# Kernel tuning notes

Hardware: AMD Instinct MI355X
Metric: run time of the kernel (lower is better)

## Reference

```python
import jax, jax.numpy as jnp
import numpy as np

N_NODES = 100_000
N_EDGES = 1_600_000
F_IN, F_HID, F_OUT = 128, 64, 128


def setup_inputs() -> dict:
    key = jax.random.key(0)
    k_x, k_e, k_w1, k_w2 = jax.random.split(key, 4)
    x = jax.random.normal(k_x, (N_NODES, F_IN), dtype=jnp.float32)
    edge_index = jax.random.randint(k_e, (2, N_EDGES), 0, N_NODES, dtype=jnp.int32)
    # Glorot-style init for the two GCN conv weight matrices
    W1 = jax.random.normal(k_w1, (F_IN, F_HID), dtype=jnp.float32) * (1.0 / np.sqrt(F_IN))
    b1 = jnp.zeros((F_HID,), dtype=jnp.float32)
    W2 = jax.random.normal(k_w2, (F_HID, F_OUT), dtype=jnp.float32) * (1.0 / np.sqrt(F_HID))
    b2 = jnp.zeros((F_OUT,), dtype=jnp.float32)
    return {"x": x, "edge_index": edge_index, "W1": W1, "b1": b1, "W2": W2, "b2": b2}


def _gcn_conv(x, W, b, src, dst, num_nodes):
    """GCNConv: out = D^{-1/2} (A + I) D^{-1/2} (x W) + b.
    Self-loops handled analytically: deg includes +1, and the self-loop
    message for node i is norm_i^2 * h_i."""
    h = x @ W  # [N, F_out]
    ones = jnp.ones(src.shape[0], dtype=h.dtype)
    deg = jax.ops.segment_sum(ones, dst, num_segments=num_nodes) + 1.0  # +1 self-loop
    norm = jax.lax.rsqrt(deg)  # [N]
    # gather source messages scaled by norm_src, scatter-add into dst
    agg = jax.ops.segment_sum(h[src] * norm[src, None], dst, num_segments=num_nodes)
    return norm[:, None] * agg + (norm * norm)[:, None] * h + b


def reference(x, edge_index, W1, b1, W2, b2):
    src, dst = edge_index[0], edge_index[1]
    n = x.shape[0]
    h = jax.nn.relu(_gcn_conv(x, W1, b1, src, dst, n))
    # dropout p=0.0 -> identity (module default)
    return _gcn_conv(h, W2, b2, src, dst, n)
```

## Files before the change

### kernel.cpp

```cpp
#include <hip/hip_runtime.h>
#include <hip/hip_bf16.h>

#define F_IN 128
#define F_HID 64
#define F_OUT 128
#define BSH 9
#define BS  (1 << BSH)
#define MAXNB 256

__device__ __forceinline__ int clampi(int v, int lo, int hi) {
    return v < lo ? lo : (v > hi ? hi : v);
}

__device__ __forceinline__ unsigned short f2bf(float f) {
    unsigned int u = __float_as_uint(f);
    u = (u + 0x7FFFu + ((u >> 16) & 1u)) >> 16;
    return (unsigned short)u;
}
__device__ __forceinline__ float bf2f(unsigned short s) {
    return __uint_as_float(((unsigned int)s) << 16);
}

__global__ void zero2_kernel(int* __restrict__ a, int* __restrict__ b, int n) {
    int i = blockIdx.x * blockDim.x + threadIdx.x;
    if (i < n) { a[i] = 0; b[i] = 0; }
}

__global__ void bhist_kernel(const int* __restrict__ dst, int* __restrict__ bhist,
                             int E, int Nn, int NB) {
    __shared__ int lh[MAXNB];
    for (int i = threadIdx.x; i < NB; i += 256) lh[i] = 0;
    __syncthreads();
    int chunk = (E + gridDim.x - 1) / gridDim.x;
    int base = blockIdx.x * chunk;
    int end = base + chunk; if (end > E) end = E;
    for (int i = base + threadIdx.x; i < end; i += 256) {
        int d = clampi(dst[i], 0, Nn - 1);
        atomicAdd(&lh[d >> BSH], 1);
    }
    __syncthreads();
    for (int i = threadIdx.x; i < NB; i += 256)
        if (lh[i]) atomicAdd(&bhist[i], lh[i]);
}

__global__ void bscan_kernel(const int* __restrict__ bhist, int* __restrict__ bbase, int NB) {
    __shared__ int s[MAXNB];
    int t = threadIdx.x;
    int v = (t < NB) ? bhist[t] : 0;
    s[t] = v;
    __syncthreads();
    for (int d = 1; d < MAXNB; d <<= 1) {
        int x = (t >= d) ? s[t - d] : 0;
        __syncthreads();
        s[t] += x;
        __syncthreads();
    }
    if (t < NB) bbase[t] = s[t] - v;
}

__global__ void bplace_kernel(const int* __restrict__ src, const int* __restrict__ dst,
                              const int* __restrict__ bbase, int* __restrict__ bcur,
                              int* __restrict__ staging, int E, int Nn, int NB) {
    __shared__ int lh[MAXNB];
    __shared__ int gb[MAXNB];
    for (int i = threadIdx.x; i < NB; i += 256) lh[i] = 0;
    __syncthreads();
    int chunk = (E + gridDim.x - 1) / gridDim.x;
    int base = blockIdx.x * chunk;
    int end = base + chunk; if (end > E) end = E;
    for (int i = base + threadIdx.x; i < end; i += 256) {
        int d = clampi(dst[i], 0, Nn - 1);
        atomicAdd(&lh[d >> BSH], 1);
    }
    __syncthreads();
    for (int i = threadIdx.x; i < NB; i += 256) {
        int c = lh[i];
        gb[i] = (c > 0) ? bbase[i] + atomicAdd(&bcur[i], c) : 0;
        lh[i] = 0;
    }
    __syncthreads();
    for (int i = base + threadIdx.x; i < end; i += 256) {
        int d = clampi(dst[i], 0, Nn - 1);
        int s = clampi(src[i], 0, Nn - 1);
        int b = d >> BSH;
        int p = gb[b] + atomicAdd(&lh[b], 1);
        staging[p] = (s << BSH) | (d & (BS - 1));
    }
}

__global__ void bfine_kernel(const int* __restrict__ bhist, const int* __restrict__ bbase,
                             const int* __restrict__ staging,
                             int* __restrict__ cnt, int* __restrict__ off,
                             float* __restrict__ nrm, int* __restrict__ csr, int Nn) {
    __shared__ int lcnt[BS];
    __shared__ int loff[BS];
    __shared__ int lcur[BS];
    __shared__ int ps[256];
    int b = blockIdx.x;
    int t = threadIdx.x;
    int base  = bbase[b];
    int count = bhist[b];
    int node0 = b << BSH;

    for (int r = t; r < BS; r += 256) lcnt[r] = 0;
    __syncthreads();
    for (int i = t; i < count; i += 256)
        atomicAdd(&lcnt[staging[base + i] & (BS - 1)], 1);
    __syncthreads();

    int a0 = lcnt[2 * t], a1 = lcnt[2 * t + 1];
    int pair = a0 + a1;
    ps[t] = pair;
    __syncthreads();
    for (int d = 1; d < 256; d <<= 1) {
        int x = (t >= d) ? ps[t - d] : 0;
        __syncthreads();
        ps[t] += x;
        __syncthreads();
    }
    int excl = ps[t] - pair;
    loff[2 * t]     = excl;
    loff[2 * t + 1] = excl + a0;
    __syncthreads();

    for (int r = t; r < BS; r += 256) {
        int node = node0 + r;
        if (node < Nn) {
            int c = lcnt[r];
            cnt[node] = c;
            off[node] = base + loff[r];
            nrm[node] = rsqrtf((float)c + 1.0f);
        }
        lcur[r] = 0;
    }
    __syncthreads();

    for (int i = t; i < count; i += 256) {
        int v = staging[base + i];
        int r = v & (BS - 1);
        int p = base + loff[r] + atomicAdd(&lcur[r], 1);
        csr[p] = v >> BSH;
    }
}

template<int K, int N, bool PRESCALE, bool BIAS, bool BF16OUT>
__global__ void gemm_tiled(const float* __restrict__ A, const float* __restrict__ B,
                           const float* __restrict__ nrm, const float* __restrict__ bias,
                           void* __restrict__ Cv, int M) {
    constexpr int CT = N / 8;
    constexpr int RB = (256 / CT) * 4;
    __shared__ float Ws[K * N];

    int tid = threadIdx.x;
    for (int i = tid; i < K * N / 4; i += 256)
        ((float4*)Ws)[i] = ((const float4*)B)[i];
    __syncthreads();

    int ct = tid % CT;
    int rt = tid / CT;
    int row0 = blockIdx.x * RB + rt * 4;
    int c0 = ct * 8;

    float acc[4][8];
#pragma unroll
    for (int r = 0; r < 4; r++)
#pragma unroll
        for (int c = 0; c < 8; c++) acc[r][c] = 0.f;

    for (int kk = 0; kk < K; kk += 8) {
        float4 av[4], av2[4];
#pragma unroll
        for (int r = 0; r < 4; r++) {
            int row = row0 + r;
            if (row < M) {
                av[r]  = *(const float4*)(A + (size_t)row * K + kk);
                av2[r] = *(const float4*)(A + (size_t)row * K + kk + 4);
            } else {
                av[r]  = make_float4(0.f, 0.f, 0.f, 0.f);
                av2[r] = make_float4(0.f, 0.f, 0.f, 0.f);
            }
        }
#pragma unroll
        for (int j = 0; j < 4; j++) {
            const float* wrow = Ws + (kk + j) * N + c0;
            float4 w0 = *(const float4*)(wrow);
            float4 w1 = *(const float4*)(wrow + 4);
            float wj[8] = {w0.x, w0.y, w0.z, w0.w, w1.x, w1.y, w1.z, w1.w};
#pragma unroll
            for (int r = 0; r < 4; r++) {
                float a = (j == 0) ? av[r].x : (j == 1) ? av[r].y : (j == 2) ? av[r].z : av[r].w;
#pragma unroll
                for (int c = 0; c < 8; c++)
                    acc[r][c] = fmaf(a, wj[c], acc[r][c]);
            }
        }
#pragma unroll
        for (int j = 0; j < 4; j++) {
            const float* wrow = Ws + (kk + 4 + j) * N + c0;
            float4 w0 = *(const float4*)(wrow);
            float4 w1 = *(const float4*)(wrow + 4);
            float wj[8] = {w0.x, w0.y, w0.z, w0.w, w1.x, w1.y, w1.z, w1.w};
#pragma unroll
            for (int r = 0; r < 4; r++) {
                float a = (j == 0) ? av2[r].x : (j == 1) ? av2[r].y : (j == 2) ? av2[r].z : av2[r].w;
#pragma unroll
                for (int c = 0; c < 8; c++)
                    acc[r][c] = fmaf(a, wj[c], acc[r][c]);
            }
        }
    }

    float bcol[8];
    if (BIAS) {
        float4 bb0 = *(const float4*)(bias + c0);
        float4 bb1 = *(const float4*)(bias + c0 + 4);
        bcol[0]=bb0.x; bcol[1]=bb0.y; bcol[2]=bb0.z; bcol[3]=bb0.w;
        bcol[4]=bb1.x; bcol[5]=bb1.y; bcol[6]=bb1.z; bcol[7]=bb1.w;
    }

#pragma unroll
    for (int r = 0; r < 4; r++) {
        int row = row0 + r;
        if (row >= M) continue;
        float scale = PRESCALE ? nrm[row] : 1.0f;
        float o[8];
#pragma unroll
        for (int c = 0; c < 8; c++) {
            float v = acc[r][c];
            if (PRESCALE) v *= scale;
            if (BIAS)     v += bcol[c];
            o[c] = v;
        }
        if (BF16OUT) {
            unsigned int pk0 = (unsigned int)f2bf(o[0]) | ((unsigned int)f2bf(o[1]) << 16);
            unsigned int pk1 = (unsigned int)f2bf(o[2]) | ((unsigned int)f2bf(o[3]) << 16);
            unsigned int pk2 = (unsigned int)f2bf(o[4]) | ((unsigned int)f2bf(o[5]) << 16);
            unsigned int pk3 = (unsigned int)f2bf(o[6]) | ((unsigned int)f2bf(o[7]) << 16);
            uint4 pk; pk.x = pk0; pk.y = pk1; pk.z = pk2; pk.w = pk3;
            *(uint4*)((unsigned short*)Cv + (size_t)row * N + c0) = pk;
        } else {
            float4 o0, o1;
            o0.x = o[0]; o0.y = o[1]; o0.z = o[2]; o0.w = o[3];
            o1.x = o[4]; o1.y = o[5]; o1.z = o[6]; o1.w = o[7];
            float* crow = (float*)Cv + (size_t)row * N + c0;
            *(float4*)(crow) = o0;
            *(float4*)(crow + 4) = o1;
        }
    }
}

template<bool CONV>
__global__ void gather64_kernel(const unsigned short* __restrict__ h,
                                const float* __restrict__ norm,
                                const int* __restrict__ off, const int* __restrict__ cnt,
                                const int* __restrict__ csr_src,
                                const float* __restrict__ bias,
                                void* __restrict__ outv, int Nn, int E) {
    int wave = (blockIdx.x * blockDim.x + threadIdx.x) >> 6;
    int lane = threadIdx.x & 63;
    int node = __builtin_amdgcn_readfirstlane(wave);
    if (node >= Nn) return;

    int o0 = __builtin_amdgcn_readfirstlane(off[node]);
    int c  = __builtin_amdgcn_readfirstlane(cnt[node]);
    if (c < 0) c = 0;
    if (o0 < 0) o0 = 0;
    if (o0 + c > E) c = E - o0;

    const int* ce = csr_src + o0;
    float sum = 0.0f;
    int e = 0;
    for (; e + 16 <= c; e += 16) {
        int si[16];
        unsigned short v[16];
#pragma unroll
        for (int u = 0; u < 16; u++) si[u] = clampi(ce[e + u], 0, Nn - 1);
#pragma unroll
        for (int u = 0; u < 16; u++) v[u] = h[(size_t)si[u] * 64 + lane];
#pragma unroll
        for (int u = 0; u < 16; u++) sum += bf2f(v[u]);
    }
    for (; e + 8 <= c; e += 8) {
        int si[8];
        unsigned short v[8];
#pragma unroll
        for (int u = 0; u < 8; u++) si[u] = clampi(ce[e + u], 0, Nn - 1);
#pragma unroll
        for (int u = 0; u < 8; u++) v[u] = h[(size_t)si[u] * 64 + lane];
#pragma unroll
        for (int u = 0; u < 8; u++) sum += bf2f(v[u]);
    }
    for (; e + 4 <= c; e += 4) {
        int si[4];
        unsigned short v[4];
#pragma unroll
        for (int u = 0; u < 4; u++) si[u] = clampi(ce[e + u], 0, Nn - 1);
#pragma unroll
        for (int u = 0; u < 4; u++) v[u] = h[(size_t)si[u] * 64 + lane];
#pragma unroll
        for (int u = 0; u < 4; u++) sum += bf2f(v[u]);
    }
    for (; e < c; e++) {
        int s = clampi(ce[e], 0, Nn - 1);
        sum += bf2f(h[(size_t)s * 64 + lane]);
    }
    float self = bf2f(h[(size_t)node * 64 + lane]);
    float nv = norm[node];
    float r = nv * (sum + self);
    if (CONV) {
        r = nv * fmaxf(r + bias[lane], 0.0f);
        ((unsigned short*)outv)[(size_t)node * 64 + lane] = f2bf(r);
    } else {
        ((float*)outv)[(size_t)node * 64 + lane] = r;
    }
}

extern "C" void kernel_launch(void* const* d_in, const int* in_sizes, int n_in,
                              void* d_out, int out_size, void* d_ws, size_t ws_size,
                              hipStream_t stream) {
    if (n_in < 6) return;
    const float* x   = (const float*)d_in[0];
    const int*   ei  = (const int*)d_in[1];
    const float* W1  = (const float*)d_in[2];
    const float* b1  = (const float*)d_in[3];
    const float* W2  = (const float*)d_in[4];
    const float* b2  = (const float*)d_in[5];
    float*       out = (float*)d_out;

    int Nn = in_sizes[0] / F_IN;
    int E  = in_sizes[1] / 2;
    const int* src = ei;
    const int* dst = ei + E;

    int NB = (Nn + BS - 1) >> BSH;
    if (NB > MAXNB) return;
    if (Nn > (1 << (31 - BSH))) return;

    size_t o = 0;
    auto alloc = [&](size_t bytes) { size_t cur = o; o += (bytes + 255) & ~(size_t)255; return cur; };
    size_t o_cnt   = alloc((size_t)Nn * 4);
    size_t o_off   = alloc((size_t)Nn * 4);
    size_t o_nrm   = alloc((size_t)Nn * 4);
    size_t o_csr   = alloc((size_t)E * 4);
    size_t o_stg   = alloc((size_t)E * 4);
    size_t o_bh    = alloc(MAXNB * 4);
    size_t o_bb    = alloc(MAXNB * 4);
    size_t o_bc    = alloc(MAXNB * 4);
    size_t o_h     = alloc((size_t)Nn * F_HID * 4);
    if (o > ws_size) return;

    char* ws = (char*)d_ws;
    int*   cnt   = (int*)(ws + o_cnt);
    int*   off   = (int*)(ws + o_off);
    float* nrm   = (float*)(ws + o_nrm);
    int*   csr   = (int*)(ws + o_csr);
    int*   stg   = (int*)(ws + o_stg);
    int*   bh    = (int*)(ws + o_bh);
    int*   bb    = (int*)(ws + o_bb);
    int*   bc    = (int*)(ws + o_bc);
    unsigned short* h1 = (unsigned short*)(ws + o_h);
    float*          q  = (float*)(ws + o_h);
    unsigned short* p  = (unsigned short*)(out + (size_t)Nn * F_HID);

    zero2_kernel<<<1, 256, 0, stream>>>(bh, bc, MAXNB);
    bhist_kernel<<<256, 256, 0, stream>>>(dst, bh, E, Nn, NB);
    bscan_kernel<<<1, 256, 0, stream>>>(bh, bb, NB);
    bplace_kernel<<<256, 256, 0, stream>>>(src, dst, bb, bc, stg, E, Nn, NB);
    bfine_kernel<<<NB, 256, 0, stream>>>(bh, bb, stg, cnt, off, nrm, csr, Nn);

    {
        constexpr int RB = (256 / (F_HID / 8)) * 4;
        gemm_tiled<F_IN, F_HID, true, false, true><<<(Nn + RB - 1) / RB, 256, 0, stream>>>(
            x, W1, nrm, nullptr, h1, Nn);
    }
    gather64_kernel<true><<<(Nn + 3) / 4, 256, 0, stream>>>(
        h1, nrm, off, cnt, csr, b1, p, Nn, E);

    gather64_kernel<false><<<(Nn + 3) / 4, 256, 0, stream>>>(
        p, nrm, off, cnt, csr, nullptr, q, Nn, E);
    {
        constexpr int RB = (256 / (F_OUT / 8)) * 4;
        gemm_tiled<F_HID, F_OUT, false, true, false><<<(Nn + RB - 1) / RB, 256, 0, stream>>>(
            q, W2, nullptr, b2, out, Nn);
    }
}
```

Before: 331.3 us.

## Fuse second-layer aggregation with W2 projection in one persistent kernel

The second gather and the following 64x128 GEMM are merged into one persistent kernel. It stages W2 in shared memory and computes each aggregated row's projection right after gathering it. This removes the fp32 intermediate write and re-read of q and one kernel launch. The cost is a 32KB shared-memory footprint per block, which limits occupancy for the latency-bound gather. The GEMM also becomes a per-node FMA loop with a fixed grid of 1024 blocks, and p moves into the workspace.

```diff
diff --git a/kernel.cpp b/kernel.cpp
--- a/kernel.cpp
+++ b/kernel.cpp
@@ -249,13 +249,12 @@
     }
 }
 
-template<bool CONV>
 __global__ void gather64_kernel(const unsigned short* __restrict__ h,
                                 const float* __restrict__ norm,
                                 const int* __restrict__ off, const int* __restrict__ cnt,
                                 const int* __restrict__ csr_src,
                                 const float* __restrict__ bias,
-                                void* __restrict__ outv, int Nn, int E) {
+                                unsigned short* __restrict__ outp, int Nn, int E) {
     int wave = (blockIdx.x * blockDim.x + threadIdx.x) >> 6;
     int lane = threadIdx.x & 63;
     int node = __builtin_amdgcn_readfirstlane(wave);
@@ -307,11 +306,104 @@
     float self = bf2f(h[(size_t)node * 64 + lane]);
     float nv = norm[node];
     float r = nv * (sum + self);
-    if (CONV) {
-        r = nv * fmaxf(r + bias[lane], 0.0f);
-        ((unsigned short*)outv)[(size_t)node * 64 + lane] = f2bf(r);
-    } else {
-        ((float*)outv)[(size_t)node * 64 + lane] = r;
+    r = nv * fmaxf(r + bias[lane], 0.0f);
+    outp[(size_t)node * 64 + lane] = f2bf(r);
+}
+
+__global__ void gather_w2_kernel(const unsigned short* __restrict__ p,
+                                 const float* __restrict__ norm,
+                                 const int* __restrict__ off, const int* __restrict__ cnt,
+                                 const int* __restrict__ csr_src,
+                                 const float* __restrict__ W2,
+                                 const float* __restrict__ b2,
+                                 float* __restrict__ out, int Nn, int E) {
+    __shared__ float W2s[F_HID * F_OUT];
+    __shared__ float qs[4][F_HID];
+
+    int tid = threadIdx.x;
+    for (int i = tid; i < F_HID * F_OUT / 4; i += 256)
+        ((float4*)W2s)[i] = ((const float4*)W2)[i];
+    __syncthreads();
+
+    int lane = tid & 63;
+    int wv   = tid >> 6;
+    int half = lane >> 5;
+    int c4   = (lane & 31) * 4;
+    int kb   = half * 32;
+
+    float4 breg = *(const float4*)(b2 + c4);
+
+    int wave0  = (blockIdx.x * blockDim.x + tid) >> 6;
+    int nwaves = (gridDim.x * blockDim.x) >> 6;
+
+    for (int node = wave0; node < Nn; node += nwaves) {
+        int un = __builtin_amdgcn_readfirstlane(node);
+        int o0 = __builtin_amdgcn_readfirstlane(off[un]);
+        int c  = __builtin_amdgcn_readfirstlane(cnt[un]);
+        if (c < 0) c = 0;
+        if (o0 < 0) o0 = 0;
+        if (o0 + c > E) c = E - o0;
+
+        const int* ce = csr_src + o0;
+        float sum = 0.0f;
+        int e = 0;
+        for (; e + 8 <= c; e += 8) {
+            int si[8];
+            unsigned short v[8];
+#pragma unroll
+            for (int u = 0; u < 8; u++) si[u] = clampi(ce[e + u], 0, Nn - 1);
+#pragma unroll
+            for (int u = 0; u < 8; u++) v[u] = p[(size_t)si[u] * 64 + lane];
+#pragma unroll
+            for (int u = 0; u < 8; u++) sum += bf2f(v[u]);
+        }
+        for (; e + 4 <= c; e += 4) {
+            int si[4];
+            unsigned short v[4];
+#pragma unroll
+            for (int u = 0; u < 4; u++) si[u] = clampi(ce[e + u], 0, Nn - 1);
+#pragma unroll
+            for (int u = 0; u < 4; u++) v[u] = p[(size_t)si[u] * 64 + lane];
+#pragma unroll
+            for (int u = 0; u < 4; u++) sum += bf2f(v[u]);
+        }
+        for (; e < c; e++) {
+            int s = clampi(ce[e], 0, Nn - 1);
+            sum += bf2f(p[(size_t)s * 64 + lane]);
+        }
+        float self = bf2f(p[(size_t)un * 64 + lane]);
+        float q = norm[un] * (sum + self);
+        qs[wv][lane] = q;
+
+        float4 acc = make_float4(0.f, 0.f, 0.f, 0.f);
+#pragma unroll
+        for (int kc = 0; kc < 32; kc += 4) {
+            float4 qv = *(const float4*)(&qs[wv][kb + kc]);
+            const float* wr = W2s + (size_t)(kb + kc) * F_OUT + c4;
+            float4 w0 = *(const float4*)(wr);
+            float4 w1 = *(const float4*)(wr + F_OUT);
+            float4 w2 = *(const float4*)(wr + 2 * F_OUT);
+            float4 w3 = *(const float4*)(wr + 3 * F_OUT);
+            acc.x = fmaf(qv.x, w0.x, acc.x); acc.y = fmaf(qv.x, w0.y, acc.y);
+            acc.z = fmaf(qv.x, w0.z, acc.z); acc.w = fmaf(qv.x, w0.w, acc.w);
+            acc.x = fmaf(qv.y, w1.x, acc.x); acc.y = fmaf(qv.y, w1.y, acc.y);
+            acc.z = fmaf(qv.y, w1.z, acc.z); acc.w = fmaf(qv.y, w1.w, acc.w);
+            acc.x = fmaf(qv.z, w2.x, acc.x); acc.y = fmaf(qv.z, w2.y, acc.y);
+            acc.z = fmaf(qv.z, w2.z, acc.z); acc.w = fmaf(qv.z, w2.w, acc.w);
+            acc.x = fmaf(qv.w, w3.x, acc.x); acc.y = fmaf(qv.w, w3.y, acc.y);
+            acc.z = fmaf(qv.w, w3.z, acc.z); acc.w = fmaf(qv.w, w3.w, acc.w);
+        }
+
+        float ox = acc.x + __shfl_down(acc.x, 32);
+        float oy = acc.y + __shfl_down(acc.y, 32);
+        float oz = acc.z + __shfl_down(acc.z, 32);
+        float ow = acc.w + __shfl_down(acc.w, 32);
+        if (half == 0) {
+            float4 o;
+            o.x = ox + breg.x; o.y = oy + breg.y;
+            o.z = oz + breg.z; o.w = ow + breg.w;
+            *(float4*)(out + (size_t)un * F_OUT + c4) = o;
+        }
     }
 }
 
@@ -359,8 +451,7 @@
     int*   bb    = (int*)(ws + o_bb);
     int*   bc    = (int*)(ws + o_bc);
     unsigned short* h1 = (unsigned short*)(ws + o_h);
-    float*          q  = (float*)(ws + o_h);
-    unsigned short* p  = (unsigned short*)(out + (size_t)Nn * F_HID);
+    unsigned short* p  = (unsigned short*)(ws + o_h + (size_t)Nn * F_HID * 2);
 
     zero2_kernel<<<1, 256, 0, stream>>>(bh, bc, MAXNB);
     bhist_kernel<<<256, 256, 0, stream>>>(dst, bh, E, Nn, NB);
@@ -373,14 +464,9 @@
         gemm_tiled<F_IN, F_HID, true, false, true><<<(Nn + RB - 1) / RB, 256, 0, stream>>>(
             x, W1, nrm, nullptr, h1, Nn);
     }
-    gather64_kernel<true><<<(Nn + 3) / 4, 256, 0, stream>>>(
+    gather64_kernel<<<(Nn + 3) / 4, 256, 0, stream>>>(
         h1, nrm, off, cnt, csr, b1, p, Nn, E);
 
-    gather64_kernel<false><<<(Nn + 3) / 4, 256, 0, stream>>>(
-        p, nrm, off, cnt, csr, nullptr, q, Nn, E);
-    {
-        constexpr int RB = (256 / (F_OUT / 8)) * 4;
-        gemm_tiled<F_HID, F_OUT, false, true, false><<<(Nn + RB - 1) / RB, 256, 0, stream>>>(
-            q, W2, nullptr, b2, out, Nn);
-    }
-}
+    gather_w2_kernel<<<1024, 256, 0, stream>>>(
+        p, nrm, off, cnt, csr, W2, b2, out, Nn, E);
+}
```

Measured after the change: 406.1 us. +22.6%, slower.
